# Optimization experiments

Measured on AMD Instinct MI355X. Metric: run time of the kernel, lower is better.

## Reference

```python
import jax, jax.numpy as jnp
import numpy as np
import math

B, N, DIM, H = 4, 2048, 1024, 16
DH = DIM // H

def setup_inputs() -> dict:
    key = jax.random.key(0)
    ks = jax.random.split(key, 7)
    return {
        "x": jax.random.normal(ks[0], (B, N, DIM), dtype=jnp.float32),
        "qkv_w": jax.random.normal(ks[1], (3 * DIM, DIM), dtype=jnp.float32) * 0.02,
        "qkv_b": jax.random.normal(ks[2], (3 * DIM,), dtype=jnp.float32) * 0.02,
        "proj_w": jax.random.normal(ks[3], (DIM, DIM), dtype=jnp.float32) * 0.02,
        "proj_b": jax.random.normal(ks[4], (DIM,), dtype=jnp.float32) * 0.02,
        "temperature": jnp.ones((1,), dtype=jnp.float32) * 0.1,
        "eps": jax.random.normal(ks[5], (B, H, N, DH), dtype=jnp.float32),
    }

def reference(x, qkv_w, qkv_b, proj_w, proj_b, temperature, eps):
    b, n, dim = x.shape
    qkv = x @ qkv_w.T + qkv_b
    qkv = qkv.reshape(b, n, 3, H, DH).transpose(2, 0, 3, 1, 4)
    q, k, v = qkv[0], qkv[1], qkv[2]
    # quantum fluctuation: additive gaussian noise on q, scaled by sigmoid(temperature)
    q = q + eps * jax.nn.sigmoid(temperature)
    scale = 1.0 / math.sqrt(DH)
    attn = jnp.einsum("bhqd,bhkd->bhqk", q, k) * scale  # [B,H,N,N]
    attn = jax.nn.softmax(attn, axis=-1)
    out = jnp.einsum("bhqk,bhkd->bhqd", attn, v)  # [B,H,N,DH]
    out = out.transpose(0, 2, 1, 3).reshape(b, n, dim)
    return out @ proj_w.T + proj_b
```

## Files before the change

kernel.cpp:

```cpp
#include <hip/hip_runtime.h>
#include <math.h>

#define B_   4
#define N_   2048
#define DIM_ 1024
#define H_   16
#define DH_  64
#define M_   (B_ * N_)
#define QKV_ELEMS ((size_t)B_ * H_ * N_ * DH_)

typedef __attribute__((ext_vector_type(8))) short short8;
typedef __attribute__((ext_vector_type(4))) float floatx4;

static __device__ inline unsigned short f2bf(float f) {
    union { float f; unsigned u; } v; v.f = f;
    unsigned r = (v.u + 0x7fffu + ((v.u >> 16) & 1u)) >> 16;
    return (unsigned short)r;
}

static __device__ inline unsigned pkbf(float a, float b) {
    unsigned ua = (__float_as_uint(a) + 0x8000u) >> 16;
    unsigned ub = (__float_as_uint(b) + 0x8000u) & 0xffff0000u;
    return ua | ub;
}

static __device__ inline void async_copy16(const void* g, void* l) {
    __builtin_amdgcn_global_load_lds(
        (const __attribute__((address_space(1))) unsigned int*)g,
        (__attribute__((address_space(3))) unsigned int*)l, 16, 0, 0);
}

__global__ __launch_bounds__(256) void f32_to_bf16_kernel(
    const float* __restrict__ src, unsigned short* __restrict__ dst, int n8)
{
    int i = blockIdx.x * 256 + threadIdx.x;
    if (i >= n8) return;
    float4 a = ((const float4*)src)[i * 2];
    float4 b = ((const float4*)src)[i * 2 + 1];
    short8 o;
    o[0] = f2bf(a.x); o[1] = f2bf(a.y); o[2] = f2bf(a.z); o[3] = f2bf(a.w);
    o[4] = f2bf(b.x); o[5] = f2bf(b.y); o[6] = f2bf(b.z); o[7] = f2bf(b.w);
    *(short8*)(dst + (size_t)i * 8) = o;
}

#define GEMM_BODY(Aptr, Bptr, K)                                               \
    __shared__ unsigned short As[2][128 * 32];                                 \
    __shared__ unsigned short Bs[2][128 * 32];                                 \
    const int tid  = threadIdx.x;                                              \
    const int lane = tid & 63;                                                 \
    const int wv   = tid >> 6;                                                 \
    const int l15  = lane & 15, quad = lane >> 4;                              \
    const int wrow = (wv >> 1) * 64, wcol = (wv & 1) * 64;                     \
    const int m0 = blockIdx.y * 128, n0 = blockIdx.x * 128;                    \
    const int lrow = lane >> 2;                                                \
    const int lkc  = (((lane & 3) ^ ((lane >> 3) & 3)) * 8); \
    const int srd  = (l15 >> 1) & 3;                    \
    const unsigned short* ga0 = Aptr + (size_t)(m0 + wv * 32 + lrow) * K + lkc;\
    const unsigned short* ga1 = ga0 + (size_t)16 * K;                          \
    const unsigned short* gb0 = Bptr + (size_t)(n0 + wv * 32 + lrow) * K + lkc;\
    const unsigned short* gb1 = gb0 + (size_t)16 * K;                          \
    floatx4 acc[4][4] = {};                                                    \
    async_copy16(ga0, &As[0][wv * 1024]);                                      \
    async_copy16(ga1, &As[0][wv * 1024 + 512]);                                \
    async_copy16(gb0, &Bs[0][wv * 1024]);                                      \
    async_copy16(gb1, &Bs[0][wv * 1024 + 512]);                                \
    for (int t = 0; t < (K) / 32; ++t) {                                       \
        const int cur = t & 1;                                                 \
        __syncthreads();              \
        if (t + 1 < (K) / 32) {                                                \
            const int k1 = (t + 1) * 32;                                       \
            async_copy16(ga0 + k1, &As[cur ^ 1][wv * 1024]);                   \
            async_copy16(ga1 + k1, &As[cur ^ 1][wv * 1024 + 512]);             \
            async_copy16(gb0 + k1, &Bs[cur ^ 1][wv * 1024]);                   \
            async_copy16(gb1 + k1, &Bs[cur ^ 1][wv * 1024 + 512]);             \
        }                                                                      \
        short8 af[4], bf[4];                                                   \
        _Pragma("unroll")                                                      \
        for (int mt = 0; mt < 4; ++mt)                                         \
            af[mt] = *(const short8*)&As[cur][(wrow + mt * 16 + l15) * 32 +    \
                                             ((quad ^ srd) * 8)];              \
        _Pragma("unroll")                                                      \
        for (int nt = 0; nt < 4; ++nt)                                         \
            bf[nt] = *(const short8*)&Bs[cur][(wcol + nt * 16 + l15) * 32 +    \
                                             ((quad ^ srd) * 8)];              \
        _Pragma("unroll")                                                      \
        for (int mt = 0; mt < 4; ++mt)                                         \
            _Pragma("unroll")                                                  \
            for (int nt = 0; nt < 4; ++nt)                                     \
                acc[mt][nt] = __builtin_amdgcn_mfma_f32_16x16x32_bf16(         \
                    af[mt], bf[nt], acc[mt][nt], 0, 0, 0);                     \
    }

__global__ __launch_bounds__(256) void gemm_qkv_bf16(
    const unsigned short* __restrict__ A, const unsigned short* __restrict__ Bm,
    const float* __restrict__ bias, const float* __restrict__ eps,
    const float* __restrict__ temp,
    unsigned short* __restrict__ qb, unsigned short* __restrict__ kb,
    unsigned short* __restrict__ vb)
{
    GEMM_BODY(A, Bm, 1024)

    const float sig = 1.0f / (1.0f + __expf(-temp[0]));
    const float qscale = 0.125f * 1.44269504f;
#pragma unroll
    for (int mt = 0; mt < 4; ++mt) {
#pragma unroll
        for (int r = 0; r < 4; ++r) {
            const int m  = m0 + wrow + mt * 16 + quad * 4 + r;
            const int b  = m >> 11;
            const int nn = m & 2047;
#pragma unroll
            for (int nt = 0; nt < 4; ++nt) {
                const int n = n0 + wcol + nt * 16 + l15;
                float val = acc[mt][nt][r] + bias[n];
                const int which = n >> 10;
                const int d  = n & 1023;
                const int h  = d >> 6;
                const int dd = d & 63;
                const size_t bh = (size_t)(b * H_ + h);
                if (which == 0) {
                    const size_t idx = (bh * N_ + nn) * DH_ + dd;
                    qb[idx] = f2bf((val + eps[idx] * sig) * qscale);
                } else if (which == 1) {
                    kb[(bh * N_ + nn) * DH_ + dd] = f2bf(val);
                } else {
                    const int kt  = nn >> 5;
                    const int k32 = nn & 31;
                    const int lo  = k32 & 15;
                    const int a   = lo >> 2;
                    const int j   = ((k32 >> 4) << 2) + (lo & 3);
                    vb[bh * (size_t)(N_ * DH_) +
                       ((size_t)(kt * 64 + dd) * 4 + a) * 8 + j] = f2bf(val);
                }
            }
        }
    }
}

__global__ __launch_bounds__(256) void gemm_proj_bf16(
    const unsigned short* __restrict__ A, const unsigned short* __restrict__ Bm,
    const float* __restrict__ bias, float* __restrict__ out)
{
    GEMM_BODY(A, Bm, 1024)

#pragma unroll
    for (int mt = 0; mt < 4; ++mt) {
#pragma unroll
        for (int r = 0; r < 4; ++r) {
            const int m = m0 + wrow + mt * 16 + quad * 4 + r;
#pragma unroll
            for (int nt = 0; nt < 4; ++nt) {
                const int n = n0 + wcol + nt * 16 + l15;
                out[(size_t)m * 1024 + n] = acc[mt][nt][r] + bias[n];
            }
        }
    }
}

__global__ __launch_bounds__(256, 2) void attn_kernel(
    const unsigned short* __restrict__ qb, const unsigned short* __restrict__ kb,
    const unsigned short* __restrict__ vt, unsigned short* __restrict__ attn_out)
{
    const int tid  = threadIdx.x;
    const int lane = tid & 63;
    const int wv   = tid >> 6;
    const int l15  = lane & 15;
    const int quad = lane >> 4;

    const int f  = blockIdx.x;
    const int L  = (f & 7) * 64 + (f >> 3);
    const int bh = L >> 3;
    const int b  = bh >> 4, h = bh & 15;
    const int qbase = (L & 7) * 256 + wv * 64;

    const unsigned short* kb_bh = kb + (size_t)bh * N_ * DH_;
    const unsigned short* vt_bh = vt + (size_t)bh * N_ * DH_;

    short8 qf[4][2];
#pragma unroll
    for (int g = 0; g < 4; ++g) {
        const unsigned short* qp =
            qb + ((size_t)bh * N_ + qbase + g * 16 + l15) * DH_;
        qf[g][0] = *(const short8*)(qp + quad * 8);
        qf[g][1] = *(const short8*)(qp + 32 + quad * 8);
    }

    floatx4 o[4][4] = {};
    float l_part[4] = {0.f, 0.f, 0.f, 0.f};

    const unsigned short* kA = kb_bh + (size_t)l15 * DH_ + quad * 8;

    short8 kfA[2][2], kfB[2][2], vfA[4], vfB[4];
    floatx4 sa0, sa1, sb0, sb1;

#define LOADK(DST, ktn)                                                        \
    do {                                                                       \
        _Pragma("unroll")                                                      \
        for (int nt = 0; nt < 2; ++nt)                                         \
            _Pragma("unroll")                                                  \
            for (int hh = 0; hh < 2; ++hh)                                     \
                DST[nt][hh] = *(const short8*)(                                \
                    kA + (size_t)((ktn) * 32 + nt * 16) * DH_ + hh * 32);      \
    } while (0)

#define LOADV(DST, ktn)                                                        \
    do {                                                                       \
        _Pragma("unroll")                                                      \
        for (int dt = 0; dt < 4; ++dt)                                         \
            DST[dt] = *(const short8*)(vt_bh +                                 \
                ((size_t)((ktn) * 64 + dt * 16 + l15) * 4 + quad) * 8);        \
    } while (0)

#define QK(S0, S1, KF, g)                                                      \
    do {                                                                       \
        floatx4 z0 = {}, z1 = {};                                              \
        z0 = __builtin_amdgcn_mfma_f32_16x16x32_bf16(KF[0][0], qf[g][0], z0, 0, 0, 0); \
        z0 = __builtin_amdgcn_mfma_f32_16x16x32_bf16(KF[0][1], qf[g][1], z0, 0, 0, 0); \
        z1 = __builtin_amdgcn_mfma_f32_16x16x32_bf16(KF[1][0], qf[g][0], z1, 0, 0, 0); \
        z1 = __builtin_amdgcn_mfma_f32_16x16x32_bf16(KF[1][1], qf[g][1], z1, 0, 0, 0); \
        S0 = z0; S1 = z1;                                                      \
    } while (0)

#define SPV(S0, S1, VF, g)                                                     \
    do {                                                                       \
        _Pragma("unroll")                                                      \
        for (int r = 0; r < 4; ++r) {                                          \
            S0[r] = __builtin_amdgcn_exp2f(S0[r]);                             \
            S1[r] = __builtin_amdgcn_exp2f(S1[r]);                             \
        }                                                                      \
        l_part[g] += ((S0[0] + S0[1]) + (S0[2] + S0[3]))                       \
                   + ((S1[0] + S1[1]) + (S1[2] + S1[3]));                      \
        union { unsigned u[4]; short8 s8; } pu;                                \
        pu.u[0] = pkbf(S0[0], S0[1]); pu.u[1] = pkbf(S0[2], S0[3]);            \
        pu.u[2] = pkbf(S1[0], S1[1]); pu.u[3] = pkbf(S1[2], S1[3]);            \
        o[g][0] = __builtin_amdgcn_mfma_f32_16x16x32_bf16(pu.s8, VF[0], o[g][0], 0, 0, 0); \
        o[g][1] = __builtin_amdgcn_mfma_f32_16x16x32_bf16(pu.s8, VF[1], o[g][1], 0, 0, 0); \
        o[g][2] = __builtin_amdgcn_mfma_f32_16x16x32_bf16(pu.s8, VF[2], o[g][2], 0, 0, 0); \
        o[g][3] = __builtin_amdgcn_mfma_f32_16x16x32_bf16(pu.s8, VF[3], o[g][3], 0, 0, 0); \
    } while (0)

    LOADK(kfA, 0); LOADV(vfA, 0);
    LOADK(kfB, 1); LOADV(vfB, 1);
    QK(sa0, sa1, kfA, 0);

    for (int kt = 0; kt < 64; kt += 2) {
        const int t2 = (kt + 2) & 63;
        const int t3 = (kt + 3) & 63;
        QK(sb0, sb1, kfA, 1);  SPV(sa0, sa1, vfA, 0);
        QK(sa0, sa1, kfA, 2);  SPV(sb0, sb1, vfA, 1);
        QK(sb0, sb1, kfA, 3);  SPV(sa0, sa1, vfA, 2);
        LOADK(kfA, t2);
        QK(sa0, sa1, kfB, 0);  SPV(sb0, sb1, vfA, 3);
        LOADV(vfA, t2);
        QK(sb0, sb1, kfB, 1);  SPV(sa0, sa1, vfB, 0);
        QK(sa0, sa1, kfB, 2);  SPV(sb0, sb1, vfB, 1);
        QK(sb0, sb1, kfB, 3);  SPV(sa0, sa1, vfB, 2);
        LOADK(kfB, t3);
        QK(sa0, sa1, kfA, 0);  SPV(sb0, sb1, vfB, 3);
        LOADV(vfB, t3);
    }
#undef QK
#undef SPV
#undef LOADK
#undef LOADV

#pragma unroll
    for (int g = 0; g < 4; ++g) {
        float lsum = l_part[g];
        lsum += __shfl_xor(lsum, 16, 64);
        lsum += __shfl_xor(lsum, 32, 64);
        const float inv = 1.0f / lsum;
#pragma unroll
        for (int r = 0; r < 4; ++r) {
            const float invq = __shfl(inv, quad * 4 + r, 64);
            const int row = qbase + g * 16 + quad * 4 + r;
#pragma unroll
            for (int dt = 0; dt < 4; ++dt)
                attn_out[((size_t)b * N_ + row) * DIM_ + h * DH_ + dt * 16 + l15] =
                    f2bf(o[g][dt][r] * invq);
        }
    }
}

extern "C" void kernel_launch(void* const* d_in, const int* in_sizes, int n_in,
                              void* d_out, int out_size, void* d_ws, size_t ws_size,
                              hipStream_t stream) {
    const float* x      = (const float*)d_in[0];
    const float* qkv_w  = (const float*)d_in[1];
    const float* qkv_b  = (const float*)d_in[2];
    const float* proj_w = (const float*)d_in[3];
    const float* proj_b = (const float*)d_in[4];
    const float* temp   = (const float*)d_in[5];
    const float* eps    = (const float*)d_in[6];
    float* out = (float*)d_out;

    unsigned short* qb   = (unsigned short*)d_ws;
    unsigned short* kb   = qb + QKV_ELEMS;
    unsigned short* vb   = kb + QKV_ELEMS;
    unsigned short* xb   = vb + QKV_ELEMS;
    unsigned short* wqb  = xb + QKV_ELEMS;
    unsigned short* pwb  = wqb + (size_t)3 * DIM_ * DIM_;
    unsigned short* attn = pwb + (size_t)DIM_ * DIM_;

    dim3 blk(256);
    f32_to_bf16_kernel<<<dim3(8388608 / 8 / 256), blk, 0, stream>>>(x, xb, 8388608 / 8);
    f32_to_bf16_kernel<<<dim3(3145728 / 8 / 256), blk, 0, stream>>>(qkv_w, wqb, 3145728 / 8);
    f32_to_bf16_kernel<<<dim3(1048576 / 8 / 256), blk, 0, stream>>>(proj_w, pwb, 1048576 / 8);

    gemm_qkv_bf16<<<dim3(24, 64), blk, 0, stream>>>(xb, wqb, qkv_b, eps, temp,
                                                    qb, kb, vb);
    attn_kernel<<<dim3(512), dim3(256), 0, stream>>>(qb, kb, vb, attn);
    gemm_proj_bf16<<<dim3(8, 64), blk, 0, stream>>>(attn, pwb, proj_b, out);
}
```

Measured before the change: 397.3 us.

## Widen GEMM tiles to 128x256 and remap blocks for XCD-aware locality

Both GEMM kernels now use 128x256 output tiles, so each wave computes 64x128 with a 4x8 MFMA accumulator array. This doubles the reuse of each A fragment and halves the grid size. The block index is also remapped with an 8-way interleave, meant to group neighbouring tiles on the same XCD for better L2 sharing. In exchange, register pressure and LDS use rise, and the proj GEMM launches only 256 blocks, which may leave CUs underfilled.

```diff
diff --git a/kernel.cpp b/kernel.cpp
--- a/kernel.cpp
+++ b/kernel.cpp
@@ -43,62 +43,68 @@
     *(short8*)(dst + (size_t)i * 8) = o;
 }
 
-#define GEMM_BODY(Aptr, Bptr, K)                                               \
+#define GEMM_BODY(Aptr, Bptr, K, M0, N0)                                       \
     __shared__ unsigned short As[2][128 * 32];                                 \
-    __shared__ unsigned short Bs[2][128 * 32];                                 \
+    __shared__ unsigned short Bs[2][256 * 32];                                 \
     const int tid  = threadIdx.x;                                              \
     const int lane = tid & 63;                                                 \
     const int wv   = tid >> 6;                                                 \
     const int l15  = lane & 15, quad = lane >> 4;                              \
-    const int wrow = (wv >> 1) * 64, wcol = (wv & 1) * 64;                     \
-    const int m0 = blockIdx.y * 128, n0 = blockIdx.x * 128;                    \
+    const int wrow = (wv >> 1) * 64, wcol = (wv & 1) * 128;                    \
+    const int m0 = (M0), n0 = (N0);                                            \
     const int lrow = lane >> 2;                                                \
     const int lkc  = (((lane & 3) ^ ((lane >> 3) & 3)) * 8); \
     const int srd  = (l15 >> 1) & 3;                    \
-    const unsigned short* ga0 = Aptr + (size_t)(m0 + wv * 32 + lrow) * K + lkc;\
-    const unsigned short* ga1 = ga0 + (size_t)16 * K;                          \
-    const unsigned short* gb0 = Bptr + (size_t)(n0 + wv * 32 + lrow) * K + lkc;\
-    const unsigned short* gb1 = gb0 + (size_t)16 * K;                          \
-    floatx4 acc[4][4] = {};                                                    \
-    async_copy16(ga0, &As[0][wv * 1024]);                                      \
-    async_copy16(ga1, &As[0][wv * 1024 + 512]);                                \
-    async_copy16(gb0, &Bs[0][wv * 1024]);                                      \
-    async_copy16(gb1, &Bs[0][wv * 1024 + 512]);                                \
+    const unsigned short* ga = Aptr + (size_t)(m0 + wv * 32 + lrow) * K + lkc; \
+    const unsigned short* gb = Bptr + (size_t)(n0 + wv * 64 + lrow) * K + lkc; \
+    floatx4 acc[4][8] = {};                                                    \
+    _Pragma("unroll")                                                          \
+    for (int c = 0; c < 2; ++c)                                                \
+        async_copy16(ga + (size_t)c * 16 * K, &As[0][wv * 1024 + c * 512]);    \
+    _Pragma("unroll")                                                          \
+    for (int c = 0; c < 4; ++c)                                                \
+        async_copy16(gb + (size_t)c * 16 * K, &Bs[0][wv * 2048 + c * 512]);    \
     for (int t = 0; t < (K) / 32; ++t) {                                       \
         const int cur = t & 1;                                                 \
-        __syncthreads();              \
+        __syncthreads();           \
         if (t + 1 < (K) / 32) {                                                \
             const int k1 = (t + 1) * 32;                                       \
-            async_copy16(ga0 + k1, &As[cur ^ 1][wv * 1024]);                   \
-            async_copy16(ga1 + k1, &As[cur ^ 1][wv * 1024 + 512]);             \
-            async_copy16(gb0 + k1, &Bs[cur ^ 1][wv * 1024]);                   \
-            async_copy16(gb1 + k1, &Bs[cur ^ 1][wv * 1024 + 512]);             \
+            _Pragma("unroll")                                                  \
+            for (int c = 0; c < 2; ++c)                                        \
+                async_copy16(ga + (size_t)c * 16 * K + k1,                     \
+                             &As[cur ^ 1][wv * 1024 + c * 512]);               \
+            _Pragma("unroll")                                                  \
+            for (int c = 0; c < 4; ++c)                                        \
+                async_copy16(gb + (size_t)c * 16 * K + k1,                     \
+                             &Bs[cur ^ 1][wv * 2048 + c * 512]);               \
         }                                                                      \
-        short8 af[4], bf[4];                                                   \
+        short8 af[4], bf[8];                                                   \
         _Pragma("unroll")                                                      \
         for (int mt = 0; mt < 4; ++mt)                                         \
             af[mt] = *(const short8*)&As[cur][(wrow + mt * 16 + l15) * 32 +    \
                                              ((quad ^ srd) * 8)];              \
         _Pragma("unroll")                                                      \
-        for (int nt = 0; nt < 4; ++nt)                                         \
+        for (int nt = 0; nt < 8; ++nt)                                         \
             bf[nt] = *(const short8*)&Bs[cur][(wcol + nt * 16 + l15) * 32 +    \
                                              ((quad ^ srd) * 8)];              \
         _Pragma("unroll")                                                      \
         for (int mt = 0; mt < 4; ++mt)                                         \
             _Pragma("unroll")                                                  \
-            for (int nt = 0; nt < 4; ++nt)                                     \
+            for (int nt = 0; nt < 8; ++nt)                                     \
                 acc[mt][nt] = __builtin_amdgcn_mfma_f32_16x16x32_bf16(         \
                     af[mt], bf[nt], acc[mt][nt], 0, 0, 0);                     \
     }
 
-__global__ __launch_bounds__(256) void gemm_qkv_bf16(
+__global__ __launch_bounds__(256, 2) void gemm_qkv_bf16(
     const unsigned short* __restrict__ A, const unsigned short* __restrict__ Bm,
     const float* __restrict__ bias, const float* __restrict__ eps,
     const float* __restrict__ temp,
     unsigned short* __restrict__ qb, unsigned short* __restrict__ kb,
     unsigned short* __restrict__ vb)
 {
-    GEMM_BODY(A, Bm, 1024)
+    const int fblk = blockIdx.y * 12 + blockIdx.x;
+    const int Lblk = (fblk & 7) * 96 + (fblk >> 3);
+    GEMM_BODY(A, Bm, 1024, (Lblk / 12) * 128, (Lblk % 12) * 256)
 
     const float sig = 1.0f / (1.0f + __expf(-temp[0]));
     const float qscale = 0.125f * 1.44269504f;
@@ -110,7 +116,7 @@
             const int b  = m >> 11;
             const int nn = m & 2047;
 #pragma unroll
-            for (int nt = 0; nt < 4; ++nt) {
+            for (int nt = 0; nt < 8; ++nt) {
                 const int n = n0 + wcol + nt * 16 + l15;
                 float val = acc[mt][nt][r] + bias[n];
                 const int which = n >> 10;
@@ -137,11 +143,13 @@
     }
 }
 
-__global__ __launch_bounds__(256) void gemm_proj_bf16(
+__global__ __launch_bounds__(256, 2) void gemm_proj_bf16(
     const unsigned short* __restrict__ A, const unsigned short* __restrict__ Bm,
     const float* __restrict__ bias, float* __restrict__ out)
 {
-    GEMM_BODY(A, Bm, 1024)
+    const int fblk = blockIdx.y * 4 + blockIdx.x;
+    const int Lblk = (fblk & 7) * 32 + (fblk >> 3);
+    GEMM_BODY(A, Bm, 1024, (Lblk >> 2) * 128, (Lblk & 3) * 256)
 
 #pragma unroll
     for (int mt = 0; mt < 4; ++mt) {
@@ -149,7 +157,7 @@
         for (int r = 0; r < 4; ++r) {
             const int m = m0 + wrow + mt * 16 + quad * 4 + r;
 #pragma unroll
-            for (int nt = 0; nt < 4; ++nt) {
+            for (int nt = 0; nt < 8; ++nt) {
                 const int n = n0 + wcol + nt * 16 + l15;
                 out[(size_t)m * 1024 + n] = acc[mt][nt][r] + bias[n];
             }
@@ -307,8 +315,8 @@
     f32_to_bf16_kernel<<<dim3(3145728 / 8 / 256), blk, 0, stream>>>(qkv_w, wqb, 3145728 / 8);
     f32_to_bf16_kernel<<<dim3(1048576 / 8 / 256), blk, 0, stream>>>(proj_w, pwb, 1048576 / 8);
 
-    gemm_qkv_bf16<<<dim3(24, 64), blk, 0, stream>>>(xb, wqb, qkv_b, eps, temp,
+    gemm_qkv_bf16<<<dim3(12, 64), blk, 0, stream>>>(xb, wqb, qkv_b, eps, temp,
                                                     qb, kb, vb);
     attn_kernel<<<dim3(512), dim3(256), 0, stream>>>(qb, kb, vb, attn);
-    gemm_proj_bf16<<<dim3(8, 64), blk, 0, stream>>>(attn, pwb, proj_b, out);
-}
+    gemm_proj_bf16<<<dim3(4, 64), blk, 0, stream>>>(attn, pwb, proj_b, out);
+}
```

Measured after the change: 421.5 us. 6.1% more time.
